# Performance work log

Hardware: AMD Instinct MI355X
Metric: run time of the kernel (lower is better)

## Reference

```python
import jax, jax.numpy as jnp
import numpy as np
from jax import lax

PAD = 40
MAX_DISP = 40
STRIDE2 = 1
CORR_MULT = 1.0


def _correlation1d(input1, input2):
    # input1, input2: [B, C, H, W]; kernel_size=1, stride1=1
    B, C, H, W = input1.shape
    D = 2 * MAX_DISP // STRIDE2 + 1  # 81 displacement channels
    # zero-pad input2 along the width dimension
    in2p = jnp.pad(input2, ((0, 0), (0, 0), (0, 0), (PAD, PAD)))
    offsets = jnp.arange(D, dtype=jnp.int32) * STRIDE2  # start col in padded map; disp = off - PAD

    def body(carry, off):
        shifted = lax.dynamic_slice(in2p, (0, 0, 0, off), (B, C, H, W))
        # mean over channels (sumelems = kernel_size^2 * C = C)
        c = jnp.sum(input1 * shifted, axis=1) / C  # [B, H, W]
        return carry, c

    _, corr = lax.scan(body, None, offsets)  # [D, B, H, W]
    out = jnp.transpose(corr, (1, 0, 2, 3)) * CORR_MULT  # [B, D, H, W]
    return out


def setup_inputs() -> dict:
    key = jax.random.key(0)
    k1, k2 = jax.random.split(key)
    input1 = jax.random.normal(k1, (8, 256, 96, 192), dtype=jnp.float32)
    input2 = jax.random.normal(k2, (8, 256, 96, 192), dtype=jnp.float32)
    return {"input1": input1, "input2": input2}


def reference(input1, input2):
    return _correlation1d(input1, input2)
```

## Files before the change

### kernel.cpp

```cpp
#include <hip/hip_runtime.h>


typedef __attribute__((ext_vector_type(8))) short short8;
typedef __attribute__((ext_vector_type(4))) float float4v;

__device__ __forceinline__ unsigned short f2bf(float f) {
  unsigned int u = __float_as_uint(f);
  return (unsigned short)((u + 0x7FFFu + ((u >> 16) & 1u)) >> 16);
}

__device__ __forceinline__ void glds4(const float* g, float* l) {
  __builtin_amdgcn_global_load_lds(
      (const __attribute__((address_space(1))) void*)g,
      (__attribute__((address_space(3))) void*)l, 4, 0, 0);
}

__global__ __launch_bounds__(256, 3) void corr1d_kernel(
    const float* __restrict__ in1, const float* __restrict__ in2,
    float* __restrict__ out) {
  constexpr int W = 192, H = 96, C = 256, D = 81;
  constexpr int HW = H * W;
  constexpr int KC = 32;
  constexpr int SR = 194;
  constexpr int ES = 196;

  __shared__ __align__(16) float smem[2 * KC * SR];
  float* As = smem;
  float* Bs = smem + KC * SR;
  float* E  = smem;

  const int bh = blockIdx.x;
  const int b = bh / H, h = bh % H;
  const int tid = threadIdx.x;
  const int lane = tid & 63;
  const int wv = tid >> 6;
  const int l15 = lane & 15, lq = lane >> 4;
  const int base = (b * C * H + h) * W;

  float4v acc[3][6];
#pragma unroll
  for (int i = 0; i < 3; ++i)
#pragma unroll
    for (int jj = 0; jj < 6; ++jj) acc[i][jj] = (float4v){0.f, 0.f, 0.f, 0.f};

  for (int m = 0; m < C / KC; ++m) {
    const int c0 = KC * m;
    __syncthreads();

#pragma unroll
    for (int r = 0; r < 8; ++r) {
      const int k = 8 * wv + r;
      const float* g1 = in1 + base + (c0 + k) * HW + lane;
      const float* g2 = in2 + base + (c0 + k) * HW + lane;
      float* lA = As + k * SR;
      float* lB = Bs + k * SR;
#pragma unroll
      for (int g = 0; g < 3; ++g) {
        glds4(g1 + 64 * g, lA + 64 * g);
        glds4(g2 + 64 * g, lB + 64 * g);
      }
    }
    __syncthreads();

    short8 af[3];
#pragma unroll
    for (int i = 0; i < 3; ++i) {
      const float* ap = As + 48 * wv + 16 * i + l15;
      unsigned short o[8];
#pragma unroll
      for (int t = 0; t < 8; ++t) o[t] = f2bf(ap[(8 * lq + t) * SR]);
      af[i] = *(const short8*)o;
    }
#pragma unroll
    for (int jt = 0; jt < 8; ++jt) {
      const int j = 16 * (3 * wv + jt) + l15;
      const bool ok = (j >= 40) && (j < 232);
      const float* bp = Bs + (ok ? (j - 40) : 0);
      unsigned short o[8];
#pragma unroll
      for (int t = 0; t < 8; ++t) {
        float v = ok ? bp[(8 * lq + t) * SR] : 0.0f;
        o[t] = f2bf(v);
      }
      short8 bfr = *(const short8*)o;
#pragma unroll
      for (int i = 0; i < 3; ++i) {
        const int jj = jt - i;
        if (jj >= 0 && jj < 6)
          acc[i][jj] = __builtin_amdgcn_mfma_f32_16x16x32_bf16(
              af[i], bfr, acc[i][jj], 0, 0, 0);
      }
    }
  }

  const float scale = 1.0f / 256.0f;
#pragma unroll
  for (int p = 0; p < 2; ++p) {
    const int dlo = p ? 41 : 0;
    const int nd  = p ? 40 : 41;
    __syncthreads();
#pragma unroll
    for (int i = 0; i < 3; ++i)
#pragma unroll
      for (int jj = 0; jj < 6; ++jj)
#pragma unroll
        for (int r = 0; r < 4; ++r) {
          const int d = 16 * jj + l15 - 4 * lq - r;
          const int w = 48 * wv + 16 * i + 4 * lq + r;
          if (d >= dlo && d < dlo + nd)
            E[(d - dlo) * ES + w] = acc[i][jj][r] * scale;
        }
    __syncthreads();
    for (int t = tid; t < nd * 48; t += 256) {
      const int dr = t / 48, g = t % 48;
      float4v val = *(const float4v*)(E + dr * ES + 4 * g);
      *(float4v*)(out + ((b * D + dlo + dr) * H + h) * W + 4 * g) = val;
    }
  }
}

extern "C" void kernel_launch(void* const* d_in, const int* in_sizes, int n_in,
                              void* d_out, int out_size, void* d_ws, size_t ws_size,
                              hipStream_t stream) {
  const float* in1 = (const float*)d_in[0];
  const float* in2 = (const float*)d_in[1];
  float* out = (float*)d_out;
  (void)in_sizes; (void)n_in; (void)out_size; (void)d_ws; (void)ws_size;
  corr1d_kernel<<<dim3(768), dim3(256), 0, stream>>>(in1, in2, out);
}
```

Measured before the change: 327.6 us.

## Double-buffer channel chunks with async LDS loads and switch to 16-deep MFMA

```diff
diff --git a/kernel.cpp b/kernel.cpp
--- a/kernel.cpp
+++ b/kernel.cpp
@@ -2,7 +2,17 @@
 
 
 typedef __attribute__((ext_vector_type(8))) short short8;
+typedef __attribute__((ext_vector_type(4))) short short4v;
 typedef __attribute__((ext_vector_type(4))) float float4v;
+
+#if defined(__has_builtin)
+#if __has_builtin(__builtin_amdgcn_mfma_f32_16x16x16bf16_1k)
+#define HAVE_MFMA16 1
+#endif
+#endif
+#ifndef HAVE_MFMA16
+#define HAVE_MFMA16 0
+#endif
 
 __device__ __forceinline__ unsigned short f2bf(float f) {
   unsigned int u = __float_as_uint(f);
@@ -20,14 +30,13 @@
     float* __restrict__ out) {
   constexpr int W = 192, H = 96, C = 256, D = 81;
   constexpr int HW = H * W;
-  constexpr int KC = 32;
+  constexpr int KC = 16;
   constexpr int SR = 194;
   constexpr int ES = 196;
-
-  __shared__ __align__(16) float smem[2 * KC * SR];
-  float* As = smem;
-  float* Bs = smem + KC * SR;
-  float* E  = smem;
+  constexpr int BUF = KC * SR;
+
+  __shared__ __align__(16) float smem[4 * BUF];
+  float* E = smem;
 
   const int bh = blockIdx.x;
   const int b = bh / H, h = bh % H;
@@ -43,13 +52,13 @@
 #pragma unroll
     for (int jj = 0; jj < 6; ++jj) acc[i][jj] = (float4v){0.f, 0.f, 0.f, 0.f};
 
-  for (int m = 0; m < C / KC; ++m) {
+  auto stage = [&](int m, int p) {
     const int c0 = KC * m;
-    __syncthreads();
-
-#pragma unroll
-    for (int r = 0; r < 8; ++r) {
-      const int k = 8 * wv + r;
+    float* As = smem + p * (2 * BUF);
+    float* Bs = As + BUF;
+#pragma unroll
+    for (int r = 0; r < 4; ++r) {
+      const int k = 4 * wv + r;
       const float* g1 = in1 + base + (c0 + k) * HW + lane;
       const float* g2 = in2 + base + (c0 + k) * HW + lane;
       float* lA = As + k * SR;
@@ -60,15 +69,54 @@
         glds4(g2 + 64 * g, lB + 64 * g);
       }
     }
-    __syncthreads();
-
+  };
+
+  auto compute_chunk = [&](int p) {
+    const float* As = smem + p * (2 * BUF);
+    const float* Bs = As + BUF;
+#if HAVE_MFMA16
+    short4v af[3];
+#pragma unroll
+    for (int i = 0; i < 3; ++i) {
+      const float* ap = As + 48 * wv + 16 * i + l15;
+      unsigned short o[4];
+#pragma unroll
+      for (int t = 0; t < 4; ++t) o[t] = f2bf(ap[(4 * lq + t) * SR]);
+      af[i] = *(const short4v*)o;
+    }
+#pragma unroll
+    for (int jt = 0; jt < 8; ++jt) {
+      const int j = 16 * (3 * wv + jt) + l15;
+      const bool ok = (j >= 40) && (j < 232);
+      const float* bp = Bs + (ok ? (j - 40) : 0);
+      unsigned short o[4];
+#pragma unroll
+      for (int t = 0; t < 4; ++t) {
+        float v = ok ? bp[(4 * lq + t) * SR] : 0.0f;
+        o[t] = f2bf(v);
+      }
+      short4v bfr = *(const short4v*)o;
+#pragma unroll
+      for (int i = 0; i < 3; ++i) {
+        const int jj = jt - i;
+        if (jj >= 0 && jj < 6)
+          acc[i][jj] = __builtin_amdgcn_mfma_f32_16x16x16bf16_1k(
+              af[i], bfr, acc[i][jj], 0, 0, 0);
+      }
+    }
+#else
+    const bool okq = (lq < 2);
+    const int rb = okq ? 8 * lq : 0;
     short8 af[3];
 #pragma unroll
     for (int i = 0; i < 3; ++i) {
       const float* ap = As + 48 * wv + 16 * i + l15;
       unsigned short o[8];
 #pragma unroll
-      for (int t = 0; t < 8; ++t) o[t] = f2bf(ap[(8 * lq + t) * SR]);
+      for (int t = 0; t < 8; ++t) {
+        float v = ap[(rb + t) * SR];
+        o[t] = okq ? f2bf(v) : (unsigned short)0;
+      }
       af[i] = *(const short8*)o;
     }
 #pragma unroll
@@ -79,8 +127,8 @@
       unsigned short o[8];
 #pragma unroll
       for (int t = 0; t < 8; ++t) {
-        float v = ok ? bp[(8 * lq + t) * SR] : 0.0f;
-        o[t] = f2bf(v);
+        float v = bp[(rb + t) * SR];
+        o[t] = (ok && okq) ? f2bf(v) : (unsigned short)0;
       }
       short8 bfr = *(const short8*)o;
 #pragma unroll
@@ -91,7 +139,31 @@
               af[i], bfr, acc[i][jj], 0, 0, 0);
       }
     }
+#endif
+  };
+
+  stage(0, 0);
+#pragma unroll 1
+  for (int t7 = 0; t7 < 7; ++t7) {
+    stage(2 * t7 + 1, 1);
+    asm volatile("s_waitcnt vmcnt(24)" ::: "memory");
+    __builtin_amdgcn_s_barrier();
+    compute_chunk(0);
+    __builtin_amdgcn_s_barrier();
+    stage(2 * t7 + 2, 0);
+    asm volatile("s_waitcnt vmcnt(24)" ::: "memory");
+    __builtin_amdgcn_s_barrier();
+    compute_chunk(1);
+    __builtin_amdgcn_s_barrier();
   }
+  stage(15, 1);
+  asm volatile("s_waitcnt vmcnt(24)" ::: "memory");
+  __builtin_amdgcn_s_barrier();
+  compute_chunk(0);
+  __builtin_amdgcn_s_barrier();
+  asm volatile("s_waitcnt vmcnt(0)" ::: "memory");
+  __builtin_amdgcn_s_barrier();
+  compute_chunk(1);
 
   const float scale = 1.0f / 256.0f;
 #pragma unroll
```

Result: no change. 325.0 us (-0.8%).
